# Kernel optimization log

Hardware: AMD Instinct MI355X
Metric: run time of the kernel (lower is better)

## Reference

```python
import jax, jax.numpy as jnp
import numpy as np

N_IN = 100_000
N_OUT = 400_000
K = 27          # 3^3 kernel offsets
C_IN = 64
C_OUT = 32


def setup_inputs() -> dict:
    key = jax.random.key(0)
    k1, k2, k3, k4 = jax.random.split(key, 4)
    feats = jax.random.normal(k1, (N_IN, C_IN), dtype=jnp.float32)
    # Minkowski-style weight: one [C_in, C_out] matrix per kernel offset
    weight = jax.random.normal(k2, (K, C_IN, C_OUT), dtype=jnp.float32) * (1.0 / np.sqrt(C_IN))
    # kernel maps: for each offset, M=N_IN (in_idx, out_idx) pairs
    in_map = jax.random.randint(k3, (K, N_IN), 0, N_IN, dtype=jnp.int64)
    out_map = jax.random.randint(k4, (K, N_IN), 0, N_OUT, dtype=jnp.int64)
    return {"feats": feats, "weight": weight, "in_map": in_map,
            "out_map": out_map, "n_out": N_OUT}


def reference(feats, weight, in_map, out_map, n_out):
    # gather-GEMM-scatter, vectorized over the K kernel offsets
    gathered = feats[in_map]                          # [K, M, C_in]
    msgs = jnp.einsum('kmc,kcd->kmd', gathered, weight)  # [K, M, C_out]
    out = jnp.zeros((n_out, msgs.shape[-1]), dtype=feats.dtype)
    out = out.at[out_map.reshape(-1)].add(msgs.reshape(-1, msgs.shape[-1]))
    return out
```

## Files before the change

kernel.cpp:

```cpp
#include <hip/hip_runtime.h>
#include <hip/hip_bf16.h>
#include <hip/hip_fp16.h>


using short8  = __attribute__((ext_vector_type(8))) short;
using floatx4 = __attribute__((ext_vector_type(4))) float;

constexpr int KOFF = 27;
constexpr int NIN  = 100000;
constexpr int NOUT = 400000;
constexpr int CIN  = 64;
constexpr int COUT = 32;
constexpr int MSGS = NIN;
constexpr int TILES = MSGS / 16;
constexpr int WPB   = 4;
constexpr int BLK_PER_K = 64;
constexpr int WSTRIDE = BLK_PER_K * WPB;

constexpr size_t ACC_BYTES   = (size_t)NOUT * COUT * 2;
constexpr size_t FEATS_BYTES = (size_t)NIN * CIN * 2;

constexpr int CVT_BLOCKS  = (NIN * CIN / 8) / 256;
constexpr int ZERO_BLOCKS = (int)(ACC_BYTES / 16) / 256;

__device__ __forceinline__ short f2bf(float f) {
    union { float f; unsigned u; } v; v.f = f;
    unsigned r = v.u + 0x7fff + ((v.u >> 16) & 1u);
    return (short)(r >> 16);
}

__global__ __launch_bounds__(256) void prep_kernel(
    const float* __restrict__ f, ushort* __restrict__ b, float4* __restrict__ accz)
{
    if (blockIdx.x < CVT_BLOCKS) {
        const int t = blockIdx.x * 256 + threadIdx.x;
        const float4* p = (const float4*)(f + (size_t)t * 8);
        float4 lo = p[0], hi = p[1];
        short8 v;
        v[0]=f2bf(lo.x); v[1]=f2bf(lo.y); v[2]=f2bf(lo.z); v[3]=f2bf(lo.w);
        v[4]=f2bf(hi.x); v[5]=f2bf(hi.y); v[6]=f2bf(hi.z); v[7]=f2bf(hi.w);
        *(short8*)(b + (size_t)t * 8) = v;
    } else {
        const int t = (blockIdx.x - CVT_BLOCKS) * 256 + threadIdx.x;
        accz[t] = make_float4(0.f, 0.f, 0.f, 0.f);
    }
}

__global__ __launch_bounds__(256) void spconv_pipe_kernel(
    const ushort* __restrict__ feats_bf,
    const float*  __restrict__ weight,
    const int*    __restrict__ in_map,
    const int*    __restrict__ out_map,
    __half2*      __restrict__ accum)
{
    const int k    = blockIdx.y;
    const int wave = threadIdx.x >> 6;
    const int lane = threadIdx.x & 63;
    const int col  = lane & 15;
    const int quad = lane >> 4;
    const long long kM = (long long)k * MSGS;

    const float* Wk = weight + k * (CIN * COUT);
    short8 bfr[2][2];
    #pragma unroll
    for (int s = 0; s < 2; ++s)
        #pragma unroll
        for (int t = 0; t < 2; ++t)
            #pragma unroll
            for (int j = 0; j < 8; ++j)
                bfr[s][t][j] = f2bf(Wk[(s * 32 + quad * 8 + j) * COUT + 2 * col + t]);

    #define LOAD_MAPS(t, inr, orow)                                   \
        {                                                             \
            const int tt = ((t) < TILES) ? (t) : (TILES - 1);         \
            const long long mb = kM + (long long)tt * 16;             \
            inr = in_map[mb + col];                                   \
            _Pragma("unroll")                                         \
            for (int i = 0; i < 4; ++i) orow[i] = out_map[mb + quad * 4 + i]; \
        }

    #define LOAD_FEATS(inr, a0, a1)                                   \
        {                                                             \
            const ushort* ar = feats_bf + (long long)(inr) * CIN;     \
            a0 = *(const short8*)(ar + quad * 8);                     \
            a1 = *(const short8*)(ar + 32 + quad * 8);                \
        }

    const int t0 = blockIdx.x * WPB + wave;

    int inrA, orowA[4];  LOAD_MAPS(t0,            inrA, orowA);
    int inrB, orowB[4];  LOAD_MAPS(t0 + WSTRIDE,  inrB, orowB);
    short8 a0A, a1A;     LOAD_FEATS(inrA, a0A, a1A);

    for (int t = t0; t < TILES; t += WSTRIDE) {
        int inrC, orowC[4];
        LOAD_MAPS(t + 2 * WSTRIDE, inrC, orowC);
        short8 a0B, a1B;
        LOAD_FEATS(inrB, a0B, a1B);

        floatx4 acc0 = {0.f, 0.f, 0.f, 0.f};
        floatx4 acc1 = {0.f, 0.f, 0.f, 0.f};
        acc0 = __builtin_amdgcn_mfma_f32_16x16x32_bf16(a0A, bfr[0][0], acc0, 0, 0, 0);
        acc1 = __builtin_amdgcn_mfma_f32_16x16x32_bf16(a0A, bfr[0][1], acc1, 0, 0, 0);
        acc0 = __builtin_amdgcn_mfma_f32_16x16x32_bf16(a1A, bfr[1][0], acc0, 0, 0, 0);
        acc1 = __builtin_amdgcn_mfma_f32_16x16x32_bf16(a1A, bfr[1][1], acc1, 0, 0, 0);

        #pragma unroll
        for (int i = 0; i < 4; ++i) {
            __half2 h = __floats2half2_rn(acc0[i], acc1[i]);
            unsafeAtomicAdd(accum + (long long)orowA[i] * 16 + col, h);
        }

        inrA = inrB; a0A = a0B; a1A = a1B;
        inrB = inrC;
        #pragma unroll
        for (int i = 0; i < 4; ++i) { orowA[i] = orowB[i]; orowB[i] = orowC[i]; }
    }
    #undef LOAD_MAPS
    #undef LOAD_FEATS
}

__global__ __launch_bounds__(256) void spconv_fp16acc_f32feats_kernel(
    const float*  __restrict__ feats_f32,
    const float*  __restrict__ weight,
    const int*    __restrict__ in_map,
    const int*    __restrict__ out_map,
    __half2*      __restrict__ accum)
{
    const int k    = blockIdx.y;
    const int wave = threadIdx.x >> 6;
    const int lane = threadIdx.x & 63;
    const int col  = lane & 15;
    const int quad = lane >> 4;
    const int tile = blockIdx.x * WPB + wave;
    if (tile >= TILES) return;
    const int m0 = tile * 16;
    const long long mapbase = (long long)k * MSGS;

    const int in_row = in_map[mapbase + m0 + col];
    int orow[4];
    #pragma unroll
    for (int i = 0; i < 4; ++i) orow[i] = out_map[mapbase + m0 + quad * 4 + i];

    const float* Wk = weight + k * (CIN * COUT);
    short8 bfr[2][2];
    #pragma unroll
    for (int s = 0; s < 2; ++s)
        #pragma unroll
        for (int t = 0; t < 2; ++t)
            #pragma unroll
            for (int j = 0; j < 8; ++j)
                bfr[s][t][j] = f2bf(Wk[(s * 32 + quad * 8 + j) * COUT + 2 * col + t]);

    const float* ar = feats_f32 + (long long)in_row * CIN + quad * 8;
    const float4* p0 = (const float4*)ar;
    const float4* p1 = (const float4*)(ar + 32);
    float4 l0 = p0[0], h0 = p0[1], l1 = p1[0], h1 = p1[1];
    short8 a0, a1;
    a0[0]=f2bf(l0.x); a0[1]=f2bf(l0.y); a0[2]=f2bf(l0.z); a0[3]=f2bf(l0.w);
    a0[4]=f2bf(h0.x); a0[5]=f2bf(h0.y); a0[6]=f2bf(h0.z); a0[7]=f2bf(h0.w);
    a1[0]=f2bf(l1.x); a1[1]=f2bf(l1.y); a1[2]=f2bf(l1.z); a1[3]=f2bf(l1.w);
    a1[4]=f2bf(h1.x); a1[5]=f2bf(h1.y); a1[6]=f2bf(h1.z); a1[7]=f2bf(h1.w);

    floatx4 acc0 = {0.f, 0.f, 0.f, 0.f};
    floatx4 acc1 = {0.f, 0.f, 0.f, 0.f};
    acc0 = __builtin_amdgcn_mfma_f32_16x16x32_bf16(a0, bfr[0][0], acc0, 0, 0, 0);
    acc1 = __builtin_amdgcn_mfma_f32_16x16x32_bf16(a0, bfr[0][1], acc1, 0, 0, 0);
    acc0 = __builtin_amdgcn_mfma_f32_16x16x32_bf16(a1, bfr[1][0], acc0, 0, 0, 0);
    acc1 = __builtin_amdgcn_mfma_f32_16x16x32_bf16(a1, bfr[1][1], acc1, 0, 0, 0);

    #pragma unroll
    for (int i = 0; i < 4; ++i) {
        __half2 h = __floats2half2_rn(acc0[i], acc1[i]);
        unsafeAtomicAdd(accum + (long long)orow[i] * 16 + col, h);
    }
}

__global__ __launch_bounds__(256) void spconv_f32atomic_kernel(
    const float* __restrict__ feats,
    const float* __restrict__ weight,
    const int*   __restrict__ in_map,
    const int*   __restrict__ out_map,
    float*       __restrict__ out)
{
    const int k    = blockIdx.y;
    const int wave = threadIdx.x >> 6;
    const int lane = threadIdx.x & 63;
    const int col  = lane & 15;
    const int quad = lane >> 4;
    const int tile = blockIdx.x * WPB + wave;
    if (tile >= TILES) return;
    const int m0 = tile * 16;
    const long long mapbase = (long long)k * MSGS;

    const float* Wk = weight + k * (CIN * COUT);
    short8 bfr[2][2];
    #pragma unroll
    for (int s = 0; s < 2; ++s)
        #pragma unroll
        for (int t = 0; t < 2; ++t)
            #pragma unroll
            for (int j = 0; j < 8; ++j)
                bfr[s][t][j] = f2bf(Wk[(s * 32 + quad * 8 + j) * COUT + t * 16 + col]);

    const int in_row = in_map[mapbase + m0 + col];
    const float* arow = feats + (long long)in_row * CIN + quad * 8;

    floatx4 acc0 = {0.f, 0.f, 0.f, 0.f};
    floatx4 acc1 = {0.f, 0.f, 0.f, 0.f};
    #pragma unroll
    for (int s = 0; s < 2; ++s) {
        const float4* p = (const float4*)(arow + s * 32);
        float4 lo = p[0], hi = p[1];
        short8 a;
        a[0]=f2bf(lo.x); a[1]=f2bf(lo.y); a[2]=f2bf(lo.z); a[3]=f2bf(lo.w);
        a[4]=f2bf(hi.x); a[5]=f2bf(hi.y); a[6]=f2bf(hi.z); a[7]=f2bf(hi.w);
        acc0 = __builtin_amdgcn_mfma_f32_16x16x32_bf16(a, bfr[s][0], acc0, 0, 0, 0);
        acc1 = __builtin_amdgcn_mfma_f32_16x16x32_bf16(a, bfr[s][1], acc1, 0, 0, 0);
    }
    #pragma unroll
    for (int i = 0; i < 4; ++i) {
        const int orow = out_map[mapbase + m0 + quad * 4 + i];
        float* po = out + (long long)orow * COUT;
        atomicAdd(po + col,      acc0[i]);
        atomicAdd(po + col + 16, acc1[i]);
    }
}

__global__ __launch_bounds__(256) void h2_to_f32_kernel(
    const __half2* __restrict__ acc, float* __restrict__ out)
{
    const int t = blockIdx.x * blockDim.x + threadIdx.x;
    const __half2* p = acc + (size_t)t * 4;
    float2 f0 = __half22float2(p[0]);
    float2 f1 = __half22float2(p[1]);
    float2 f2 = __half22float2(p[2]);
    float2 f3 = __half22float2(p[3]);
    float4* o = (float4*)out + (size_t)t * 2;
    o[0] = make_float4(f0.x, f0.y, f1.x, f1.y);
    o[1] = make_float4(f2.x, f2.y, f3.x, f3.y);
}

extern "C" void kernel_launch(void* const* d_in, const int* in_sizes, int n_in,
                              void* d_out, int out_size, void* d_ws, size_t ws_size,
                              hipStream_t stream) {
    const float* feats   = (const float*)d_in[0];
    const float* weight  = (const float*)d_in[1];
    const int*   in_map  = (const int*)d_in[2];
    const int*   out_map = (const int*)d_in[3];
    float*       out     = (float*)d_out;

    if (ws_size >= ACC_BYTES + FEATS_BYTES) {
        __half2* accum    = (__half2*)d_ws;
        ushort*  feats_bf = (ushort*)((char*)d_ws + ACC_BYTES);

        prep_kernel<<<CVT_BLOCKS + ZERO_BLOCKS, 256, 0, stream>>>(
            feats, feats_bf, (float4*)accum);
        spconv_pipe_kernel<<<dim3(BLK_PER_K, KOFF), 256, 0, stream>>>(
            feats_bf, weight, in_map, out_map, accum);
        h2_to_f32_kernel<<<(NOUT * 16 / 4) / 256, 256, 0, stream>>>(accum, out);
    } else if (ws_size >= ACC_BYTES) {
        __half2* accum = (__half2*)d_ws;
        hipMemsetAsync(accum, 0, ACC_BYTES, stream);
        spconv_fp16acc_f32feats_kernel<<<dim3((TILES + WPB - 1) / WPB, KOFF), 256, 0, stream>>>(
            feats, weight, in_map, out_map, accum);
        h2_to_f32_kernel<<<(NOUT * 16 / 4) / 256, 256, 0, stream>>>(accum, out);
    } else {
        hipMemsetAsync(d_out, 0, (size_t)out_size * sizeof(float), stream);
        spconv_f32atomic_kernel<<<dim3((TILES + WPB - 1) / WPB, KOFF), 256, 0, stream>>>(
            feats, weight, in_map, out_map, out);
    }
}
```

Measured before the change: 256.4 us.

## Deepen gather prefetch pipeline, double blocks per offset, add nontemporal memory hints

Result: no change. 253.8 us, median of 2 (-1.0%).

```diff
diff --git a/kernel.cpp b/kernel.cpp
--- a/kernel.cpp
+++ b/kernel.cpp
@@ -5,6 +5,8 @@
 
 using short8  = __attribute__((ext_vector_type(8))) short;
 using floatx4 = __attribute__((ext_vector_type(4))) float;
+using f32x4   = __attribute__((ext_vector_type(4))) float;
+using i32x4   = __attribute__((ext_vector_type(4))) int;
 
 constexpr int KOFF = 27;
 constexpr int NIN  = 100000;
@@ -14,7 +16,7 @@
 constexpr int MSGS = NIN;
 constexpr int TILES = MSGS / 16;
 constexpr int WPB   = 4;
-constexpr int BLK_PER_K = 64;
+constexpr int BLK_PER_K = 128;
 constexpr int WSTRIDE = BLK_PER_K * WPB;
 
 constexpr size_t ACC_BYTES   = (size_t)NOUT * COUT * 2;
@@ -30,19 +32,21 @@
 }
 
 __global__ __launch_bounds__(256) void prep_kernel(
-    const float* __restrict__ f, ushort* __restrict__ b, float4* __restrict__ accz)
+    const float* __restrict__ f, ushort* __restrict__ b, f32x4* __restrict__ accz)
 {
     if (blockIdx.x < CVT_BLOCKS) {
         const int t = blockIdx.x * 256 + threadIdx.x;
-        const float4* p = (const float4*)(f + (size_t)t * 8);
-        float4 lo = p[0], hi = p[1];
+        const f32x4* p = (const f32x4*)(f + (size_t)t * 8);
+        f32x4 lo = __builtin_nontemporal_load(p);
+        f32x4 hi = __builtin_nontemporal_load(p + 1);
         short8 v;
-        v[0]=f2bf(lo.x); v[1]=f2bf(lo.y); v[2]=f2bf(lo.z); v[3]=f2bf(lo.w);
-        v[4]=f2bf(hi.x); v[5]=f2bf(hi.y); v[6]=f2bf(hi.z); v[7]=f2bf(hi.w);
+        v[0]=f2bf(lo[0]); v[1]=f2bf(lo[1]); v[2]=f2bf(lo[2]); v[3]=f2bf(lo[3]);
+        v[4]=f2bf(hi[0]); v[5]=f2bf(hi[1]); v[6]=f2bf(hi[2]); v[7]=f2bf(hi[3]);
         *(short8*)(b + (size_t)t * 8) = v;
     } else {
         const int t = (blockIdx.x - CVT_BLOCKS) * 256 + threadIdx.x;
-        accz[t] = make_float4(0.f, 0.f, 0.f, 0.f);
+        f32x4 z = {0.f, 0.f, 0.f, 0.f};
+        __builtin_nontemporal_store(z, accz + t);
     }
 }
 
@@ -58,7 +62,7 @@
     const int lane = threadIdx.x & 63;
     const int col  = lane & 15;
     const int quad = lane >> 4;
-    const long long kM = (long long)k * MSGS;
+    const int kM   = k * MSGS;
 
     const float* Wk = weight + k * (CIN * COUT);
     short8 bfr[2][2];
@@ -70,33 +74,31 @@
             for (int j = 0; j < 8; ++j)
                 bfr[s][t][j] = f2bf(Wk[(s * 32 + quad * 8 + j) * COUT + 2 * col + t]);
 
-    #define LOAD_MAPS(t, inr, orow)                                   \
-        {                                                             \
-            const int tt = ((t) < TILES) ? (t) : (TILES - 1);         \
-            const long long mb = kM + (long long)tt * 16;             \
-            inr = in_map[mb + col];                                   \
-            _Pragma("unroll")                                         \
-            for (int i = 0; i < 4; ++i) orow[i] = out_map[mb + quad * 4 + i]; \
-        }
-
-    #define LOAD_FEATS(inr, a0, a1)                                   \
-        {                                                             \
-            const ushort* ar = feats_bf + (long long)(inr) * CIN;     \
-            a0 = *(const short8*)(ar + quad * 8);                     \
-            a1 = *(const short8*)(ar + 32 + quad * 8);                \
-        }
+    auto load_maps = [&](int t, int& inr, i32x4& orow) {
+        const int tt = (t < TILES) ? t : (TILES - 1);
+        const int mb = kM + tt * 16;
+        inr  = __builtin_nontemporal_load(in_map + mb + col);
+        orow = __builtin_nontemporal_load((const i32x4*)(out_map + mb + quad * 4));
+    };
+    auto load_feats = [&](int inr, short8& a0, short8& a1) {
+        const ushort* ar = feats_bf + inr * CIN;
+        a0 = *(const short8*)(ar + quad * 8);
+        a1 = *(const short8*)(ar + 32 + quad * 8);
+    };
 
     const int t0 = blockIdx.x * WPB + wave;
 
-    int inrA, orowA[4];  LOAD_MAPS(t0,            inrA, orowA);
-    int inrB, orowB[4];  LOAD_MAPS(t0 + WSTRIDE,  inrB, orowB);
-    short8 a0A, a1A;     LOAD_FEATS(inrA, a0A, a1A);
+    int inrA; i32x4 orowA; load_maps(t0,               inrA, orowA);
+    int inrB; i32x4 orowB; load_maps(t0 +     WSTRIDE, inrB, orowB);
+    int inrC; i32x4 orowC; load_maps(t0 + 2 * WSTRIDE, inrC, orowC);
+    short8 a0A, a1A; load_feats(inrA, a0A, a1A);
+    short8 a0B, a1B; load_feats(inrB, a0B, a1B);
 
     for (int t = t0; t < TILES; t += WSTRIDE) {
-        int inrC, orowC[4];
-        LOAD_MAPS(t + 2 * WSTRIDE, inrC, orowC);
-        short8 a0B, a1B;
-        LOAD_FEATS(inrB, a0B, a1B);
+        int inrD; i32x4 orowD;
+        load_maps(t + 3 * WSTRIDE, inrD, orowD);
+        short8 a0C, a1C;
+        load_feats(inrC, a0C, a1C);
 
         floatx4 acc0 = {0.f, 0.f, 0.f, 0.f};
         floatx4 acc1 = {0.f, 0.f, 0.f, 0.f};
@@ -105,19 +107,17 @@
         acc0 = __builtin_amdgcn_mfma_f32_16x16x32_bf16(a1A, bfr[1][0], acc0, 0, 0, 0);
         acc1 = __builtin_amdgcn_mfma_f32_16x16x32_bf16(a1A, bfr[1][1], acc1, 0, 0, 0);
 
+        const int orr[4] = {orowA[0], orowA[1], orowA[2], orowA[3]};
         #pragma unroll
         for (int i = 0; i < 4; ++i) {
             __half2 h = __floats2half2_rn(acc0[i], acc1[i]);
-            unsafeAtomicAdd(accum + (long long)orowA[i] * 16 + col, h);
+            unsafeAtomicAdd(accum + orr[i] * 16 + col, h);
         }
 
-        inrA = inrB; a0A = a0B; a1A = a1B;
-        inrB = inrC;
-        #pragma unroll
-        for (int i = 0; i < 4; ++i) { orowA[i] = orowB[i]; orowB[i] = orowC[i]; }
-    }
-    #undef LOAD_MAPS
-    #undef LOAD_FEATS
+        inrA = inrB; a0A = a0B; a1A = a1B; orowA = orowB;
+        inrB = inrC; a0B = a0C; a1B = a1C; orowB = orowC;
+        inrC = inrD; orowC = orowD;
+    }
 }
 
 __global__ __launch_bounds__(256) void spconv_fp16acc_f32feats_kernel(
@@ -236,9 +236,11 @@
     float2 f1 = __half22float2(p[1]);
     float2 f2 = __half22float2(p[2]);
     float2 f3 = __half22float2(p[3]);
-    float4* o = (float4*)out + (size_t)t * 2;
-    o[0] = make_float4(f0.x, f0.y, f1.x, f1.y);
-    o[1] = make_float4(f2.x, f2.y, f3.x, f3.y);
+    f32x4* o = (f32x4*)out + (size_t)t * 2;
+    f32x4 o0 = {f0.x, f0.y, f1.x, f1.y};
+    f32x4 o1 = {f2.x, f2.y, f3.x, f3.y};
+    __builtin_nontemporal_store(o0, o);
+    __builtin_nontemporal_store(o1, o + 1);
 }
 
 extern "C" void kernel_launch(void* const* d_in, const int* in_sizes, int n_in,
@@ -255,7 +257,7 @@
         ushort*  feats_bf = (ushort*)((char*)d_ws + ACC_BYTES);
 
         prep_kernel<<<CVT_BLOCKS + ZERO_BLOCKS, 256, 0, stream>>>(
-            feats, feats_bf, (float4*)accum);
+            feats, feats_bf, (f32x4*)accum);
         spconv_pipe_kernel<<<dim3(BLK_PER_K, KOFF), 256, 0, stream>>>(
             feats_bf, weight, in_map, out_map, accum);
         h2_to_f32_kernel<<<(NOUT * 16 / 4) / 256, 256, 0, stream>>>(accum, out);
```
